# Optimization experiments

Hardware: AMD Instinct MI355X
Metric: run time of the kernel (lower is better)

Reference implementation:

```python
import jax, jax.numpy as jnp
import numpy as np

RANK = 4
IN_FEATURES = 1024
OUT_FEATURES = 1024
ALPHA = 1.0
SCALING = ALPHA / RANK


def setup_inputs() -> dict:
    key = jax.random.key(0)
    kx, ka = jax.random.split(key)
    x = jax.random.normal(kx, (4, 8192, IN_FEATURES), dtype=jnp.float32)
    # kaiming_uniform_(a=sqrt(5)) on [rank, in_features]: bound = sqrt(3) * gain / sqrt(fan_in)
    # gain = sqrt(2/(1+a^2)) = sqrt(1/3); fan_in = in_features -> bound = 1/sqrt(in_features)
    bound = 1.0 / np.sqrt(IN_FEATURES)
    lora_A = jax.random.uniform(ka, (RANK, IN_FEATURES), dtype=jnp.float32, minval=-bound, maxval=bound)
    # original init is zeros for B; use random values so the output/gradients are non-trivial
    lora_B = jax.random.normal(jax.random.fold_in(key, 7), (OUT_FEATURES, RANK), dtype=jnp.float32) * 0.02
    return {"x": x, "lora_A": lora_A, "lora_B": lora_B}


def reference(x, lora_A, lora_B):
    # h = scaling * (x @ A^T) @ B^T   (dropout p=0 -> identity)
    h = jnp.einsum('bsi,ri->bsr', x, lora_A)      # [B, S, rank]
    h = jnp.einsum('bsr,or->bso', h, lora_B)      # [B, S, out_features]
    return h * SCALING
```

## Files before the change

### kernel.cpp

```cpp
#include <hip/hip_runtime.h>
#include <stdint.h>

#define IN_F 1024
#define OUT_F 1024
#define SCALING 0.25f
#define TILE_ROWS 16
#define BLOCK 256

__global__ __launch_bounds__(BLOCK, 3) void lora_tile(
    const float* __restrict__ x, const float* __restrict__ A,
    const float* __restrict__ B, float* __restrict__ out, int nrows) {
  __shared__ float4 hf[TILE_ROWS];

  const int t = threadIdx.x;
  const int lane = t & 63;
  const int wave = t >> 6;
  const int row0 = blockIdx.x * TILE_ROWS;
  if (row0 >= nrows) return;

  const float4* __restrict__ A4 = (const float4*)A;
  float4 a[4][4];
#pragma unroll
  for (int r = 0; r < 4; ++r)
#pragma unroll
    for (int k = 0; k < 4; ++k) a[r][k] = A4[r * 256 + lane + 64 * k];

  const float4* __restrict__ x4 =
      (const float4*)(x + (size_t)(row0 + wave * 4) * IN_F);

  float4 xr[2][4];
#pragma unroll
  for (int k = 0; k < 4; ++k) xr[0][k] = x4[lane + 64 * k];

#pragma unroll
  for (int i = 0; i < 4; ++i) {
    if (i + 1 < 4) {
#pragma unroll
      for (int k = 0; k < 4; ++k)
        xr[(i + 1) & 1][k] = x4[(i + 1) * 256 + lane + 64 * k];
    }
    float p0 = 0.f, p1 = 0.f, p2 = 0.f, p3 = 0.f;
#pragma unroll
    for (int k = 0; k < 4; ++k) {
      const float4 xv = xr[i & 1][k];
      p0 += xv.x * a[0][k].x + xv.y * a[0][k].y + xv.z * a[0][k].z +
            xv.w * a[0][k].w;
      p1 += xv.x * a[1][k].x + xv.y * a[1][k].y + xv.z * a[1][k].z +
            xv.w * a[1][k].w;
      p2 += xv.x * a[2][k].x + xv.y * a[2][k].y + xv.z * a[2][k].z +
            xv.w * a[2][k].w;
      p3 += xv.x * a[3][k].x + xv.y * a[3][k].y + xv.z * a[3][k].z +
            xv.w * a[3][k].w;
    }
#pragma unroll
    for (int off = 1; off < 64; off <<= 1) {
      p0 += __shfl_xor(p0, off, 64);
      p1 += __shfl_xor(p1, off, 64);
      p2 += __shfl_xor(p2, off, 64);
      p3 += __shfl_xor(p3, off, 64);
    }
    if (lane == 0)
      hf[wave * 4 + i] = make_float4(p0 * SCALING, p1 * SCALING, p2 * SCALING,
                                     p3 * SCALING);
  }
  __syncthreads();

  const float4* __restrict__ B4 = (const float4*)B;
  const float4 bf0 = B4[4 * t + 0];
  const float4 bf1 = B4[4 * t + 1];
  const float4 bf2 = B4[4 * t + 2];
  const float4 bf3 = B4[4 * t + 3];

  float4* __restrict__ out4 = (float4*)out;
#pragma unroll
  for (int r = 0; r < TILE_ROWS; ++r) {
    const float4 h = hf[r];
    float4 res;
    res.x = h.x * bf0.x + h.y * bf0.y + h.z * bf0.z + h.w * bf0.w;
    res.y = h.x * bf1.x + h.y * bf1.y + h.z * bf1.z + h.w * bf1.w;
    res.z = h.x * bf2.x + h.y * bf2.y + h.z * bf2.z + h.w * bf2.w;
    res.w = h.x * bf3.x + h.y * bf3.y + h.z * bf3.z + h.w * bf3.w;
    out4[(size_t)(row0 + r) * (OUT_F / 4) + t] = res;
  }
}

extern "C" void kernel_launch(void* const* d_in, const int* in_sizes, int n_in,
                              void* d_out, int out_size, void* d_ws,
                              size_t ws_size, hipStream_t stream) {
  const float* x = (const float*)d_in[0];
  const float* A = (const float*)d_in[1];
  const float* B = (const float*)d_in[2];
  float* out = (float*)d_out;

  const int nrows = in_sizes[0] / IN_F;
  const int blocks = (nrows + TILE_ROWS - 1) / TILE_ROWS;
  lora_tile<<<blocks, BLOCK, 0, stream>>>(x, A, B, out, nrows);
}
```

Before: 232.5 us.

## Split LoRA into two kernels through a workspace buffer, with fused fallback

Splits the fused kernel into two kernels that run whenever a large enough workspace is supplied. The first computes the rank-4 projection h for 8 rows per wave and writes it to the workspace. The second expands h through B into the output using non-temporal stores. A new fused kernel keeping B in registers is used only when no workspace is available. The split is meant to let each phase run at full occupancy and streaming bandwidth, at the cost of a second launch and a small round trip of h through memory.

```diff
diff --git a/kernel.cpp b/kernel.cpp
--- a/kernel.cpp
+++ b/kernel.cpp
@@ -4,45 +4,139 @@
 #define IN_F 1024
 #define OUT_F 1024
 #define SCALING 0.25f
-#define TILE_ROWS 16
-#define BLOCK 256
 
-__global__ __launch_bounds__(BLOCK, 3) void lora_tile(
+typedef float f32x4 __attribute__((ext_vector_type(4)));
+
+#define PIN4(v) asm volatile("" : "+v"((v).x), "+v"((v).y), "+v"((v).z), "+v"((v).w))
+
+__global__ __launch_bounds__(256) void lora_h(
     const float* __restrict__ x, const float* __restrict__ A,
-    const float* __restrict__ B, float* __restrict__ out, int nrows) {
-  __shared__ float4 hf[TILE_ROWS];
+    float* __restrict__ h, int nrows) {
+  const int lane = threadIdx.x & 63;
+  const int gw = (int)((blockIdx.x * 256u + threadIdx.x) >> 6);
+  const int row_base = gw * 8;
+  if (row_base >= nrows) return;
 
-  const int t = threadIdx.x;
-  const int lane = t & 63;
-  const int wave = t >> 6;
-  const int row0 = blockIdx.x * TILE_ROWS;
-  if (row0 >= nrows) return;
+  const float4* __restrict__ X4 = (const float4*)x;
+  const float4* __restrict__ A4 = (const float4*)A;
 
-  const float4* __restrict__ A4 = (const float4*)A;
   float4 a[4][4];
 #pragma unroll
   for (int r = 0; r < 4; ++r)
 #pragma unroll
     for (int k = 0; k < 4; ++k) a[r][k] = A4[r * 256 + lane + 64 * k];
-
-  const float4* __restrict__ x4 =
-      (const float4*)(x + (size_t)(row0 + wave * 4) * IN_F);
+#pragma unroll
+  for (int r = 0; r < 4; ++r)
+#pragma unroll
+    for (int k = 0; k < 4; ++k) PIN4(a[r][k]);
 
   float4 xr[2][4];
+  {
+    const size_t r0 = (size_t)row_base * 256;
 #pragma unroll
-  for (int k = 0; k < 4; ++k) xr[0][k] = x4[lane + 64 * k];
+    for (int k = 0; k < 4; ++k) xr[0][k] = X4[r0 + lane + 64 * k];
+  }
 
+  float4* __restrict__ h4 = (float4*)h;
 #pragma unroll
-  for (int i = 0; i < 4; ++i) {
-    if (i + 1 < 4) {
+  for (int it = 0; it < 8; ++it) {
+    const int row = row_base + it;
+    if (it + 1 < 8) {
+      const int prow = min(row_base + it + 1, nrows - 1);
+      const size_t rp = (size_t)prow * 256;
 #pragma unroll
-      for (int k = 0; k < 4; ++k)
-        xr[(i + 1) & 1][k] = x4[(i + 1) * 256 + lane + 64 * k];
+      for (int k = 0; k < 4; ++k) xr[(it + 1) & 1][k] = X4[rp + lane + 64 * k];
     }
+    if (row < nrows) {
+      float p0 = 0.f, p1 = 0.f, p2 = 0.f, p3 = 0.f;
+#pragma unroll
+      for (int k = 0; k < 4; ++k) {
+        const float4 xv = xr[it & 1][k];
+        p0 += xv.x * a[0][k].x + xv.y * a[0][k].y + xv.z * a[0][k].z +
+              xv.w * a[0][k].w;
+        p1 += xv.x * a[1][k].x + xv.y * a[1][k].y + xv.z * a[1][k].z +
+              xv.w * a[1][k].w;
+        p2 += xv.x * a[2][k].x + xv.y * a[2][k].y + xv.z * a[2][k].z +
+              xv.w * a[2][k].w;
+        p3 += xv.x * a[3][k].x + xv.y * a[3][k].y + xv.z * a[3][k].z +
+              xv.w * a[3][k].w;
+      }
+#pragma unroll
+      for (int off = 1; off < 64; off <<= 1) {
+        p0 += __shfl_xor(p0, off, 64);
+        p1 += __shfl_xor(p1, off, 64);
+        p2 += __shfl_xor(p2, off, 64);
+        p3 += __shfl_xor(p3, off, 64);
+      }
+      if (lane == 0)
+        h4[row] = make_float4(p0 * SCALING, p1 * SCALING, p2 * SCALING,
+                              p3 * SCALING);
+    }
+  }
+}
+
+__global__ __launch_bounds__(256) void lora_out(
+    const float* __restrict__ h, const float* __restrict__ B,
+    float* __restrict__ out, int nrows) {
+  __shared__ float hs[64 * 4];
+  const int t = threadIdx.x;
+  const int base = blockIdx.x * 64;
+  if (base >= nrows) return;
+
+  const float4* __restrict__ B4 = (const float4*)B;
+  const float4 b0 = B4[4 * t + 0];
+  const float4 b1 = B4[4 * t + 1];
+  const float4 b2 = B4[4 * t + 2];
+  const float4 b3 = B4[4 * t + 3];
+
+  const int tile = min(64, nrows - base);
+  if (t < tile * 4) hs[t] = h[base * 4 + t];
+  __syncthreads();
+
+  f32x4* __restrict__ out4 = (f32x4*)out;
+  const float4* __restrict__ hv = (const float4*)hs;
+#pragma unroll 4
+  for (int r = 0; r < tile; ++r) {
+    const float4 hh = hv[r];
+    f32x4 res;
+    res.x = hh.x * b0.x + hh.y * b0.y + hh.z * b0.z + hh.w * b0.w;
+    res.y = hh.x * b1.x + hh.y * b1.y + hh.z * b1.z + hh.w * b1.w;
+    res.z = hh.x * b2.x + hh.y * b2.y + hh.z * b2.z + hh.w * b2.w;
+    res.w = hh.x * b3.x + hh.y * b3.y + hh.z * b3.z + hh.w * b3.w;
+    __builtin_nontemporal_store(res, &out4[(size_t)(base + r) * 256 + t]);
+  }
+}
+
+__global__ __launch_bounds__(256) void lora_fused(
+    const float* __restrict__ x, const float* __restrict__ A,
+    const float* __restrict__ B, float* __restrict__ out, int nrows) {
+  const int lane = threadIdx.x & 63;
+  const int gw = (int)((blockIdx.x * 256u + threadIdx.x) >> 6);
+  const int row_base = gw * 4;
+  if (row_base >= nrows) return;
+
+  const float4* __restrict__ X4 = (const float4*)x;
+  const float4* __restrict__ A4 = (const float4*)A;
+  const float4* __restrict__ B4 = (const float4*)B;
+  float4* __restrict__ out4 = (float4*)out;
+
+  float4 a[4][4], b[4][4];
+#pragma unroll
+  for (int r = 0; r < 4; ++r)
+#pragma unroll
+    for (int k = 0; k < 4; ++k) a[r][k] = A4[r * 256 + lane + 64 * k];
+#pragma unroll
+  for (int k = 0; k < 4; ++k)
+#pragma unroll
+    for (int c = 0; c < 4; ++c) b[k][c] = B4[4 * (lane + 64 * k) + c];
+
+  for (int it = 0; it < 4; ++it) {
+    const int row = row_base + it;
+    if (row >= nrows) break;
     float p0 = 0.f, p1 = 0.f, p2 = 0.f, p3 = 0.f;
 #pragma unroll
     for (int k = 0; k < 4; ++k) {
-      const float4 xv = xr[i & 1][k];
+      const float4 xv = X4[(size_t)row * 256 + lane + 64 * k];
       p0 += xv.x * a[0][k].x + xv.y * a[0][k].y + xv.z * a[0][k].z +
             xv.w * a[0][k].w;
       p1 += xv.x * a[1][k].x + xv.y * a[1][k].y + xv.z * a[1][k].z +
@@ -59,28 +153,17 @@
       p2 += __shfl_xor(p2, off, 64);
       p3 += __shfl_xor(p3, off, 64);
     }
-    if (lane == 0)
-      hf[wave * 4 + i] = make_float4(p0 * SCALING, p1 * SCALING, p2 * SCALING,
-                                     p3 * SCALING);
-  }
-  __syncthreads();
-
-  const float4* __restrict__ B4 = (const float4*)B;
-  const float4 bf0 = B4[4 * t + 0];
-  const float4 bf1 = B4[4 * t + 1];
-  const float4 bf2 = B4[4 * t + 2];
-  const float4 bf3 = B4[4 * t + 3];
-
-  float4* __restrict__ out4 = (float4*)out;
+    const float h0 = p0 * SCALING, h1 = p1 * SCALING, h2 = p2 * SCALING,
+                h3 = p3 * SCALING;
 #pragma unroll
-  for (int r = 0; r < TILE_ROWS; ++r) {
-    const float4 h = hf[r];
-    float4 res;
-    res.x = h.x * bf0.x + h.y * bf0.y + h.z * bf0.z + h.w * bf0.w;
-    res.y = h.x * bf1.x + h.y * bf1.y + h.z * bf1.z + h.w * bf1.w;
-    res.z = h.x * bf2.x + h.y * bf2.y + h.z * bf2.z + h.w * bf2.w;
-    res.w = h.x * bf3.x + h.y * bf3.y + h.z * bf3.z + h.w * bf3.w;
-    out4[(size_t)(row0 + r) * (OUT_F / 4) + t] = res;
+    for (int k = 0; k < 4; ++k) {
+      float4 res;
+      res.x = h0 * b[k][0].x + h1 * b[k][0].y + h2 * b[k][0].z + h3 * b[k][0].w;
+      res.y = h0 * b[k][1].x + h1 * b[k][1].y + h2 * b[k][1].z + h3 * b[k][1].w;
+      res.z = h0 * b[k][2].x + h1 * b[k][2].y + h2 * b[k][2].z + h3 * b[k][2].w;
+      res.w = h0 * b[k][3].x + h1 * b[k][3].y + h2 * b[k][3].z + h3 * b[k][3].w;
+      out4[(size_t)row * 256 + lane + 64 * k] = res;
+    }
   }
 }
 
@@ -93,6 +176,16 @@
   float* out = (float*)d_out;
 
   const int nrows = in_sizes[0] / IN_F;
-  const int blocks = (nrows + TILE_ROWS - 1) / TILE_ROWS;
-  lora_tile<<<blocks, BLOCK, 0, stream>>>(x, A, B, out, nrows);
+  const size_t h_bytes = (size_t)nrows * 4 * sizeof(float);
+
+  if (d_ws != nullptr && ws_size >= h_bytes) {
+    float* h = (float*)d_ws;
+    const int b1 = (nrows + 31) / 32;
+    lora_h<<<b1, 256, 0, stream>>>(x, A, h, nrows);
+    const int b2 = (nrows + 63) / 64;
+    lora_out<<<b2, 256, 0, stream>>>(h, B, out, nrows);
+  } else {
+    const int b = (nrows + 15) / 16;
+    lora_fused<<<b, 256, 0, stream>>>(x, A, B, out, nrows);
+  }
 }
```

After: 236.4 us. No clear change (+1.7%).

## Fuse per-wave LoRA rows with a deep register prefetch ring and nontemporal stores

Applied to the files above, without the earlier changes.

Each wave now handles 16 rows end to end. A 4-deep register ring prefetches x rows ahead of the reduction, and the second projection runs straight from registers with B held per lane. This removes the shared-memory handoff and the block barrier, and output is written with nontemporal stores. The cost is much higher register pressure, enforced by asm pinning and a lower occupancy bound (2 blocks instead of 3), plus 4x fewer blocks.

```diff
diff --git a/kernel.cpp b/kernel.cpp
--- a/kernel.cpp
+++ b/kernel.cpp
@@ -4,45 +4,66 @@
 #define IN_F 1024
 #define OUT_F 1024
 #define SCALING 0.25f
-#define TILE_ROWS 16
 #define BLOCK 256
+#define RPW 16
+#define DEPTH 4
 
-__global__ __launch_bounds__(BLOCK, 3) void lora_tile(
+typedef float f32x4 __attribute__((ext_vector_type(4)));
+
+#define PIN4(v) \
+  asm volatile("" : "+v"((v).x), "+v"((v).y), "+v"((v).z), "+v"((v).w))
+
+__global__ __launch_bounds__(BLOCK, 2) void lora_fused(
     const float* __restrict__ x, const float* __restrict__ A,
     const float* __restrict__ B, float* __restrict__ out, int nrows) {
-  __shared__ float4 hf[TILE_ROWS];
+  const int lane = threadIdx.x & 63;
+  const int gw = (int)((blockIdx.x * (unsigned)BLOCK + threadIdx.x) >> 6);
+  const int row_base = gw * RPW;
+  if (row_base >= nrows) return;
+  const int last = nrows - 1;
 
-  const int t = threadIdx.x;
-  const int lane = t & 63;
-  const int wave = t >> 6;
-  const int row0 = blockIdx.x * TILE_ROWS;
-  if (row0 >= nrows) return;
+  const float4* __restrict__ X4 = (const float4*)x;
+  const float4* __restrict__ A4 = (const float4*)A;
+  const float4* __restrict__ B4 = (const float4*)B;
+  f32x4* __restrict__ out4 = (f32x4*)out;
 
-  const float4* __restrict__ A4 = (const float4*)A;
   float4 a[4][4];
 #pragma unroll
   for (int r = 0; r < 4; ++r)
 #pragma unroll
     for (int k = 0; k < 4; ++k) a[r][k] = A4[r * 256 + lane + 64 * k];
 
-  const float4* __restrict__ x4 =
-      (const float4*)(x + (size_t)(row0 + wave * 4) * IN_F);
-
-  float4 xr[2][4];
+  float4 b[4][4];
 #pragma unroll
-  for (int k = 0; k < 4; ++k) xr[0][k] = x4[lane + 64 * k];
+  for (int k = 0; k < 4; ++k)
+#pragma unroll
+    for (int c = 0; c < 4; ++c) b[k][c] = B4[4 * (lane + 64 * k) + c];
 
 #pragma unroll
-  for (int i = 0; i < 4; ++i) {
-    if (i + 1 < 4) {
+  for (int r = 0; r < 4; ++r)
 #pragma unroll
-      for (int k = 0; k < 4; ++k)
-        xr[(i + 1) & 1][k] = x4[(i + 1) * 256 + lane + 64 * k];
-    }
+    for (int k = 0; k < 4; ++k) PIN4(a[r][k]);
+#pragma unroll
+  for (int k = 0; k < 4; ++k)
+#pragma unroll
+    for (int c = 0; c < 4; ++c) PIN4(b[k][c]);
+
+  float4 ring[DEPTH][4];
+#pragma unroll
+  for (int d = 0; d < DEPTH; ++d) {
+    const size_t rr = (size_t)min(row_base + d, last) * 256;
+#pragma unroll
+    for (int k = 0; k < 4; ++k) ring[d][k] = X4[rr + lane + 64 * k];
+  }
+
+#pragma unroll
+  for (int i = 0; i < RPW; ++i) {
+    const int slot = i & (DEPTH - 1);
+
     float p0 = 0.f, p1 = 0.f, p2 = 0.f, p3 = 0.f;
 #pragma unroll
     for (int k = 0; k < 4; ++k) {
-      const float4 xv = xr[i & 1][k];
+      const float4 xv = ring[slot][k];
       p0 += xv.x * a[0][k].x + xv.y * a[0][k].y + xv.z * a[0][k].z +
             xv.w * a[0][k].w;
       p1 += xv.x * a[1][k].x + xv.y * a[1][k].y + xv.z * a[1][k].z +
@@ -52,6 +73,13 @@
       p3 += xv.x * a[3][k].x + xv.y * a[3][k].y + xv.z * a[3][k].z +
             xv.w * a[3][k].w;
     }
+
+    if (i + DEPTH < RPW) {
+      const size_t rr = (size_t)min(row_base + i + DEPTH, last) * 256;
+#pragma unroll
+      for (int k = 0; k < 4; ++k) ring[slot][k] = X4[rr + lane + 64 * k];
+    }
+
 #pragma unroll
     for (int off = 1; off < 64; off <<= 1) {
       p0 += __shfl_xor(p0, off, 64);
@@ -59,28 +87,26 @@
       p2 += __shfl_xor(p2, off, 64);
       p3 += __shfl_xor(p3, off, 64);
     }
-    if (lane == 0)
-      hf[wave * 4 + i] = make_float4(p0 * SCALING, p1 * SCALING, p2 * SCALING,
-                                     p3 * SCALING);
-  }
-  __syncthreads();
 
-  const float4* __restrict__ B4 = (const float4*)B;
-  const float4 bf0 = B4[4 * t + 0];
-  const float4 bf1 = B4[4 * t + 1];
-  const float4 bf2 = B4[4 * t + 2];
-  const float4 bf3 = B4[4 * t + 3];
-
-  float4* __restrict__ out4 = (float4*)out;
+    const int row = row_base + i;
+    if (row < nrows) {
+      const float h0 = p0 * SCALING, h1 = p1 * SCALING, h2 = p2 * SCALING,
+                  h3 = p3 * SCALING;
+      const size_t orow = (size_t)row * 256;
 #pragma unroll
-  for (int r = 0; r < TILE_ROWS; ++r) {
-    const float4 h = hf[r];
-    float4 res;
-    res.x = h.x * bf0.x + h.y * bf0.y + h.z * bf0.z + h.w * bf0.w;
-    res.y = h.x * bf1.x + h.y * bf1.y + h.z * bf1.z + h.w * bf1.w;
-    res.z = h.x * bf2.x + h.y * bf2.y + h.z * bf2.z + h.w * bf2.w;
-    res.w = h.x * bf3.x + h.y * bf3.y + h.z * bf3.z + h.w * bf3.w;
-    out4[(size_t)(row0 + r) * (OUT_F / 4) + t] = res;
+      for (int k = 0; k < 4; ++k) {
+        f32x4 res;
+        res.x = h0 * b[k][0].x + h1 * b[k][0].y + h2 * b[k][0].z +
+                h3 * b[k][0].w;
+        res.y = h0 * b[k][1].x + h1 * b[k][1].y + h2 * b[k][1].z +
+                h3 * b[k][1].w;
+        res.z = h0 * b[k][2].x + h1 * b[k][2].y + h2 * b[k][2].z +
+                h3 * b[k][2].w;
+        res.w = h0 * b[k][3].x + h1 * b[k][3].y + h2 * b[k][3].z +
+                h3 * b[k][3].w;
+        __builtin_nontemporal_store(res, &out4[orow + lane + 64 * k]);
+      }
+    }
   }
 }
 
@@ -93,6 +119,7 @@
   float* out = (float*)d_out;
 
   const int nrows = in_sizes[0] / IN_F;
-  const int blocks = (nrows + TILE_ROWS - 1) / TILE_ROWS;
-  lora_tile<<<blocks, BLOCK, 0, stream>>>(x, A, B, out, nrows);
+  const int rows_per_block = RPW * (BLOCK / 64);
+  const int blocks = (nrows + rows_per_block - 1) / rows_per_block;
+  lora_fused<<<blocks, BLOCK, 0, stream>>>(x, A, B, out, nrows);
 }
```

After: 243.4 us. 1.05x slower.
